# Kernel tuning notes

Measured on AMD Instinct MI355X. Metric: run time of the kernel, lower is better.

Reference implementation:

```python
import jax, jax.numpy as jnp
import numpy as np

N_NODES, N_EDGES, N_ROOTS = 32768, 131072, 1024
VOCAB, EMB_D, FEAT = 50000, 256, 128
SEQ, HEADS, OUT_CH = 16, 16, 125
KERNELS = (5, 6, 7, 8)


def _add_self_loops(edge_index, n):
    loop = jnp.arange(n, dtype=edge_index.dtype)
    src = jnp.concatenate([edge_index[0], loop])
    dst = jnp.concatenate([edge_index[1], loop])
    return src, dst


def _gat_conv(x, W, a_src, a_dst, b, src, dst, n):
    # PyG GATConv (heads=1): h=xW, e_ij = LeakyReLU(a_s.h_j + a_d.h_i), softmax over incoming edges of i
    h = x @ W                                   # [N, F]
    al_s = h @ a_src                            # [N]
    al_d = h @ a_dst                            # [N]
    e = jax.nn.leaky_relu(al_s[src] + al_d[dst], 0.2)   # [E+N]
    m = jax.ops.segment_max(e, dst, num_segments=n)
    ex = jnp.exp(e - m[dst])
    den = jax.ops.segment_sum(ex, dst, num_segments=n)
    coef = ex / den[dst]
    out = jax.ops.segment_sum(coef[:, None] * h[src], dst, num_segments=n)
    return out + b


def _gcn_conv(x, W, b, src, dst, n):
    h = x @ W
    ones = jnp.ones_like(src, dtype=x.dtype)
    deg = jax.ops.segment_sum(ones, dst, num_segments=n)
    dinv = jax.lax.rsqrt(jnp.maximum(deg, 1.0))
    norm = dinv[src] * dinv[dst]                # [E+N]
    out = jax.ops.segment_sum(norm[:, None] * h[src], dst, num_segments=n)
    return out + b


def _transformer_block(x, Wq, bq, Wk, bk, Wv, bv, Wo, bo, g, be):
    # multi-head self-attention + output proj + residual + layernorm (attn_dropout=0)
    n, s, d = x.shape
    dh = d // HEADS
    q = (x @ Wq + bq).reshape(n, s, HEADS, dh)
    k = (x @ Wk + bk).reshape(n, s, HEADS, dh)
    v = (x @ Wv + bv).reshape(n, s, HEADS, dh)
    att = jnp.einsum('nqhd,nkhd->nhqk', q, k) / np.sqrt(dh).astype(np.float32)
    att = jax.nn.softmax(att, axis=-1)
    o = jnp.einsum('nhqk,nkhd->nqhd', att, v).reshape(n, s, d)
    o = o @ Wo + bo
    y = x + o
    mu = jnp.mean(y, axis=-1, keepdims=True)
    var = jnp.var(y, axis=-1, keepdims=True)
    return (y - mu) * jax.lax.rsqrt(var + 1e-5) * g + be


def _conv_branch(t, ws, bs):
    # t: [N, D, S]; Conv1d VALID + ReLU + max-pool over full output length
    feats = []
    for w, b in zip(ws, bs):
        a = jax.lax.conv_general_dilated(t, w, (1,), 'VALID',
                                         dimension_numbers=('NCH', 'OIH', 'NCH'))
        a = jax.nn.relu(a + b[:, None])
        feats.append(jnp.max(a, axis=-1))       # [N, OUT_CH]
    return jnp.concatenate(feats, axis=1)        # [N, 4*OUT_CH]


def _forward(x2, emb, Wq, bq, Wk, bk, Wv, bv, Wo, bo, ln_g, ln_b,
             gat1_W, gat1_as, gat1_ad, gat1_b, gcn1_W, gcn1_b,
             gat2_W, gat2_as, gat2_ad, gat2_b, gcn2_W, gcn2_b,
             conv_w0, conv_b0, conv_w1, conv_b1, conv_w2, conv_b2, conv_w3, conv_b3,
             fc1_W, fc1_b, fc2_W, fc2_b,
             text2, edge_index, root_index, rootpost_index):
    n = x2.shape[0]
    src, dst = _add_self_loops(edge_index, n)

    stance_graph = _gat_conv(x2, gat1_W, gat1_as, gat1_ad, gat1_b, src, dst, n)
    stance_shared = _gcn_conv(x2, gcn1_W, gcn1_b, src, dst, n)

    t = emb[text2]                                            # [N, S, D]
    t = _transformer_block(t, Wq, bq, Wk, bk, Wv, bv, Wo, bo, ln_g, ln_b)
    t_avg = jnp.mean(t, axis=1)                               # [N, D]

    cat = jnp.concatenate([stance_graph, stance_shared, t_avg], axis=1)  # [N, 2F+D]
    stance_graph2 = _gat_conv(cat, gat2_W, gat2_as, gat2_ad, gat2_b, src, dst, n)
    _ = _gcn_conv(stance_shared, gcn2_W, gcn2_b, src, dst, n)  # computed but unused in forward (faithful)

    tc = jnp.transpose(t, (0, 2, 1))                          # [N, D, S]
    text_feat = _conv_branch(tc, (conv_w0, conv_w1, conv_w2, conv_w3),
                             (conv_b0, conv_b1, conv_b2, conv_b3))  # [N, 500]

    final = jnp.concatenate([stance_graph2[root_index],
                             text_feat[root_index],
                             text_feat[rootpost_index]], axis=1)     # [B, F+1000]
    h = jax.nn.relu(final @ fc1_W + fc1_b)
    return h @ fc2_W + fc2_b                                  # [B, 3]


def setup_inputs() -> dict:
    key = jax.random.key(0)
    ks = iter(jax.random.split(key, 48))
    s = 0.05
    inp = {}
    inp['x2'] = jax.random.normal(next(ks), (N_NODES, FEAT), jnp.float32)
    inp['emb'] = jax.random.normal(next(ks), (VOCAB, EMB_D), jnp.float32) * s
    for nm in ['Wq', 'Wk', 'Wv', 'Wo']:
        inp[nm] = jax.random.normal(next(ks), (EMB_D, EMB_D), jnp.float32) * s
    for nm in ['bq', 'bk', 'bv', 'bo']:
        inp[nm] = jnp.zeros((EMB_D,), jnp.float32)
    inp['ln_g'] = jnp.ones((EMB_D,), jnp.float32)
    inp['ln_b'] = jnp.zeros((EMB_D,), jnp.float32)
    inp['gat1_W'] = jax.random.normal(next(ks), (FEAT, FEAT), jnp.float32) * s
    inp['gat1_as'] = jax.random.normal(next(ks), (FEAT,), jnp.float32) * s
    inp['gat1_ad'] = jax.random.normal(next(ks), (FEAT,), jnp.float32) * s
    inp['gat1_b'] = jnp.zeros((FEAT,), jnp.float32)
    inp['gcn1_W'] = jax.random.normal(next(ks), (FEAT, FEAT), jnp.float32) * s
    inp['gcn1_b'] = jnp.zeros((FEAT,), jnp.float32)
    inp['gat2_W'] = jax.random.normal(next(ks), (2 * FEAT + EMB_D, FEAT), jnp.float32) * s
    inp['gat2_as'] = jax.random.normal(next(ks), (FEAT,), jnp.float32) * s
    inp['gat2_ad'] = jax.random.normal(next(ks), (FEAT,), jnp.float32) * s
    inp['gat2_b'] = jnp.zeros((FEAT,), jnp.float32)
    inp['gcn2_W'] = jax.random.normal(next(ks), (FEAT, FEAT), jnp.float32) * s
    inp['gcn2_b'] = jnp.zeros((FEAT,), jnp.float32)
    for i, K in enumerate(KERNELS):
        inp[f'conv_w{i}'] = jax.random.normal(next(ks), (OUT_CH, EMB_D, K), jnp.float32) * s
        inp[f'conv_b{i}'] = jnp.zeros((OUT_CH,), jnp.float32)
    inp['fc1_W'] = jax.random.normal(next(ks), (FEAT + 8 * OUT_CH, 300), jnp.float32) * s
    inp['fc1_b'] = jnp.zeros((300,), jnp.float32)
    inp['fc2_W'] = jax.random.normal(next(ks), (300, 3), jnp.float32) * s
    inp['fc2_b'] = jnp.zeros((3,), jnp.float32)
    inp['text2'] = jax.random.randint(next(ks), (N_NODES, SEQ), 0, VOCAB, jnp.int32)
    inp['edge_index'] = jax.random.randint(next(ks), (2, N_EDGES), 0, N_NODES, jnp.int32)
    inp['root_index'] = jax.random.randint(next(ks), (N_ROOTS,), 0, N_NODES, jnp.int32)
    inp['rootpost_index'] = jax.random.randint(next(ks), (N_ROOTS,), 0, N_NODES, jnp.int32)
    return inp


def reference(x2, emb, Wq, bq, Wk, bk, Wv, bv, Wo, bo, ln_g, ln_b,
              gat1_W, gat1_as, gat1_ad, gat1_b, gcn1_W, gcn1_b,
              gat2_W, gat2_as, gat2_ad, gat2_b, gcn2_W, gcn2_b,
              conv_w0, conv_b0, conv_w1, conv_b1, conv_w2, conv_b2, conv_w3, conv_b3,
              fc1_W, fc1_b, fc2_W, fc2_b,
              text2, edge_index, root_index, rootpost_index):
    return _forward(x2, emb, Wq, bq, Wk, bk, Wv, bv, Wo, bo, ln_g, ln_b,
                    gat1_W, gat1_as, gat1_ad, gat1_b, gcn1_W, gcn1_b,
                    gat2_W, gat2_as, gat2_ad, gat2_b, gcn2_W, gcn2_b,
                    conv_w0, conv_b0, conv_w1, conv_b1, conv_w2, conv_b2, conv_w3, conv_b3,
                    fc1_W, fc1_b, fc2_W, fc2_b,
                    text2, edge_index, root_index, rootpost_index)
```

## Files before the change

kernel.cpp:

```cpp
#include <hip/hip_runtime.h>
#include <hip/hip_bf16.h>
#include <cstdint>
#include <cstddef>

#define N_NODES 32768
#define N_EDGES 131072
#define ET_EDGES (N_EDGES + N_NODES)
#define N_ROOTS 1024
#define EMB_D 256
#define FEAT 128
#define SEQ 16
#define OUT_CH 125

static inline int cdiv(long long a, long long b) { return (int)((a + b - 1) / b); }

typedef short short8 __attribute__((ext_vector_type(8)));
typedef short short4v __attribute__((ext_vector_type(4)));
typedef float f32x4 __attribute__((ext_vector_type(4)));

__device__ __forceinline__ float warpReduceSum(float v) {
#pragma unroll
    for (int m = 32; m; m >>= 1) v += __shfl_xor(v, m, 64);
    return v;
}
__device__ __forceinline__ int encf(float f) {
    int i = __float_as_int(f);
    return i >= 0 ? i : (i ^ 0x7fffffff);
}
__device__ __forceinline__ float decf(int i) {
    return __int_as_float(i >= 0 ? i : (i ^ 0x7fffffff));
}
__device__ __forceinline__ short f2bs(float x) {
    unsigned u = __float_as_uint(x);
    u += 0x7fffu + ((u >> 16) & 1u);
    return (short)(u >> 16);
}
__device__ __forceinline__ short2 f2bs2(float a, float b) {
    union {
        __hip_bfloat162 h;
        short2 s;
    } u;
    u.h = __float22bfloat162_rn(make_float2(a, b));
    return u.s;
}
__device__ __forceinline__ float bs2f(short s) {
    return __uint_as_float(((unsigned)(unsigned short)s) << 16);
}

__global__ void fill_i32(int* p, int v, int n) {
    int i = blockIdx.x * 256 + threadIdx.x;
    if (i < n) p[i] = v;
}

__global__ void init_cat(float* __restrict__ cat, const float* __restrict__ b1, const float* __restrict__ b2) {
    int i = blockIdx.x * 256 + threadIdx.x;
    int n = i >> 8, c = i & 255;
    float b = (c < 128) ? b1[c] : b2[c - 128];
    cat[(size_t)n * 512 + c] = b;
}

__global__ void repack_wall(const float* __restrict__ cw0, const float* __restrict__ cw1,
                            const float* __restrict__ cw2, const float* __restrict__ cw3,
                            __hip_bfloat16* __restrict__ wall) {
    int i = blockIdx.x * 256 + threadIdx.x;
    if (i >= 512 * 2048) return;
    int r = i >> 11, c = i & 2047;
    int k = c >> 8, ic = c & 255;
    float v = 0.f;
    if (r < 500) {
        int Kidx = r / 125, oc = r - Kidx * 125;
        int K = 5 + Kidx;
        if (k < K) {
            const float* cw = Kidx == 0 ? cw0 : Kidx == 1 ? cw1 : Kidx == 2 ? cw2 : cw3;
            v = cw[((size_t)oc * 256 + ic) * K + k];
        }
    }
    wall[i] = __float2bfloat16(v);
}

__global__ void repack_xf(const float* __restrict__ Wq, const float* __restrict__ Wk, const float* __restrict__ Wv,
                          const float* __restrict__ Wo, const float* __restrict__ bq, const float* __restrict__ bk,
                          const float* __restrict__ bv, short* __restrict__ wqkvT, short* __restrict__ woT,
                          float* __restrict__ bqkv) {
    int i = blockIdx.x * 256 + threadIdx.x;
    if (i < 768 * 256) {
        int n = i >> 8, k = i & 255;
        const float* W = n < 256 ? Wq : n < 512 ? Wk : Wv;
        wqkvT[i] = f2bs(W[k * 256 + (n & 255)]);
    }
    if (i < 256 * 256) {
        int n = i >> 8, k = i & 255;
        woT[i] = f2bs(Wo[k * 256 + n]);
    }
    if (i < 768) bqkv[i] = i < 256 ? bq[i] : i < 512 ? bk[i - 256] : bv[i - 512];
}

__global__ void repack_wT(const float* __restrict__ W, short* __restrict__ out, int K, int N) {
    int i = blockIdx.x * 256 + threadIdx.x;
    if (i >= K * N) return;
    int n = i / K, k = i - n * K;
    out[i] = f2bs(W[(size_t)k * N + n]);
}

__global__ __launch_bounds__(256) void mfma_gemm_n128(const float* __restrict__ A, const short* __restrict__ Wt,
                                                      float* __restrict__ C, int K) {
    __shared__ short As[128 * 40];
    __shared__ short Bs[128 * 40];
    const int m0 = blockIdx.x * 128;
    const int tid = threadIdx.x;
    const int lane = tid & 63;
    const int wave = tid >> 6;
    const int wm = (wave >> 1) * 64, wn = (wave & 1) * 64;
    const int quad = lane >> 4, l16 = lane & 15;

    const int r0 = tid >> 2, kc = (tid & 3) * 8;
    const int r1 = r0 + 64;

    f32x4 acc[4][4];
#pragma unroll
    for (int i = 0; i < 4; i++)
#pragma unroll
        for (int j = 0; j < 4; j++) acc[i][j] = (f32x4){0.f, 0.f, 0.f, 0.f};

    for (int k0 = 0; k0 < K; k0 += 32) {
#pragma unroll
        for (int rr = 0; rr < 2; rr++) {
            const int r = rr ? r1 : r0;
            const float* pa = A + (size_t)(m0 + r) * K + k0 + kc;
            float4 a0 = ((const float4*)pa)[0], a1 = ((const float4*)pa)[1];
            short2 c0 = f2bs2(a0.x, a0.y), c1 = f2bs2(a0.z, a0.w), c2 = f2bs2(a1.x, a1.y), c3 = f2bs2(a1.z, a1.w);
            *(short8*)(As + r * 40 + kc) = (short8){c0.x, c0.y, c1.x, c1.y, c2.x, c2.y, c3.x, c3.y};
        }
        *(short8*)(Bs + r0 * 40 + kc) = *(const short8*)(Wt + (size_t)r0 * K + k0 + kc);
        *(short8*)(Bs + r1 * 40 + kc) = *(const short8*)(Wt + (size_t)r1 * K + k0 + kc);
        __syncthreads();
        short8 af[4], bfr[4];
#pragma unroll
        for (int i = 0; i < 4; i++) af[i] = *(const short8*)(As + (wm + i * 16 + l16) * 40 + quad * 8);
#pragma unroll
        for (int j = 0; j < 4; j++) bfr[j] = *(const short8*)(Bs + (wn + j * 16 + l16) * 40 + quad * 8);
#pragma unroll
        for (int i = 0; i < 4; i++)
#pragma unroll
            for (int j = 0; j < 4; j++)
                acc[i][j] = __builtin_amdgcn_mfma_f32_16x16x32_bf16(af[i], bfr[j], acc[i][j], 0, 0, 0);
        __syncthreads();
    }
#pragma unroll
    for (int i = 0; i < 4; i++) {
#pragma unroll
        for (int j = 0; j < 4; j++) {
            const int col = wn + j * 16 + l16;
            const size_t base = (size_t)(m0 + wm + i * 16 + quad * 4) * 128 + col;
#pragma unroll
            for (int r = 0; r < 4; r++) C[base + (size_t)r * 128] = acc[i][j][r];
        }
    }
}

__global__ __launch_bounds__(256) void gemm64(const float* __restrict__ A, const float* __restrict__ B,
                                              const float* __restrict__ bias, float* __restrict__ C,
                                              int M, int N, int K, int lda, int ldc, int doRelu) {
    __shared__ float As[16][65];
    __shared__ float Bs[16][65];
    const int bm = blockIdx.y * 64, bn = blockIdx.x * 64;
    const int tid = threadIdx.x;
    const int tx = tid & 15, ty = tid >> 4;
    float acc[4][4] = {};
    for (int k0 = 0; k0 < K; k0 += 16) {
#pragma unroll
        for (int j = 0; j < 4; j++) {
            int i = tid + j * 256;
            int kk = i & 15, m = i >> 4;
            int gr = bm + m, gc = k0 + kk;
            As[kk][m] = (gr < M && gc < K) ? A[(size_t)gr * lda + gc] : 0.f;
        }
#pragma unroll
        for (int j = 0; j < 4; j++) {
            int i = tid + j * 256;
            int n = i & 63, kk = i >> 6;
            int gr = k0 + kk, gc = bn + n;
            Bs[kk][n] = (gr < K && gc < N) ? B[(size_t)gr * N + gc] : 0.f;
        }
        __syncthreads();
#pragma unroll
        for (int kk = 0; kk < 16; kk++) {
            float a[4], b[4];
#pragma unroll
            for (int i2 = 0; i2 < 4; i2++) a[i2] = As[kk][ty * 4 + i2];
#pragma unroll
            for (int j2 = 0; j2 < 4; j2++) b[j2] = Bs[kk][tx * 4 + j2];
#pragma unroll
            for (int i2 = 0; i2 < 4; i2++)
#pragma unroll
                for (int j2 = 0; j2 < 4; j2++) acc[i2][j2] = fmaf(a[i2], b[j2], acc[i2][j2]);
        }
        __syncthreads();
    }
#pragma unroll
    for (int i2 = 0; i2 < 4; i2++) {
        int r = bm + ty * 4 + i2;
        if (r >= M) continue;
#pragma unroll
        for (int j2 = 0; j2 < 4; j2++) {
            int c = bn + tx * 4 + j2;
            if (c >= N) continue;
            float v = acc[i2][j2];
            if (bias) v += bias[c];
            if (doRelu) v = fmaxf(v, 0.f);
            C[(size_t)r * ldc + c] = v;
        }
    }
}

__global__ __launch_bounds__(256) void alpha_kernel(const float* __restrict__ h, const float* __restrict__ asrc,
                                                    const float* __restrict__ adst, float* __restrict__ als,
                                                    float* __restrict__ ald) {
    int gw = (blockIdx.x * 256 + threadIdx.x) >> 6;
    int lane = threadIdx.x & 63;
    if (gw >= N_NODES) return;
    const float* row = h + (size_t)gw * FEAT;
    float v0 = row[lane], v1 = row[lane + 64];
    float ps = v0 * asrc[lane] + v1 * asrc[lane + 64];
    float pd = v0 * adst[lane] + v1 * adst[lane + 64];
    ps = warpReduceSum(ps);
    pd = warpReduceSum(pd);
    if (lane == 0) {
        als[gw] = ps;
        ald[gw] = pd;
    }
}

__device__ __forceinline__ void edge_decode(int i, const int* __restrict__ ei, int& s, int& d) {
    if (i < N_EDGES) {
        s = ei[i];
        d = ei[N_EDGES + i];
    } else {
        s = d = i - N_EDGES;
    }
}

__global__ void edge_p1(const int* __restrict__ ei, const float* __restrict__ als, const float* __restrict__ ald,
                        float* __restrict__ elog, int* __restrict__ menc, float* dega) {
    int i = blockIdx.x * 256 + threadIdx.x;
    if (i >= ET_EDGES) return;
    int s, d;
    edge_decode(i, ei, s, d);
    float e = als[s] + ald[d];
    e = (e >= 0.f) ? e : 0.2f * e;
    elog[i] = e;
    atomicMax(&menc[d], encf(e));
    if (dega) unsafeAtomicAdd(&dega[d], 1.f);
}

__global__ void edge_p2(const int* __restrict__ ei, float* __restrict__ elog, const int* __restrict__ menc,
                        float* __restrict__ den) {
    int i = blockIdx.x * 256 + threadIdx.x;
    if (i >= ET_EDGES) return;
    int s, d;
    edge_decode(i, ei, s, d);
    float ex = __expf(elog[i] - decf(menc[d]));
    elog[i] = ex;
    unsafeAtomicAdd(&den[d], ex);
}

__global__ void edge_p2b(const int* __restrict__ ei, float* __restrict__ elog, const float* __restrict__ den) {
    int i = blockIdx.x * 256 + threadIdx.x;
    if (i >= ET_EDGES) return;
    int s, d;
    edge_decode(i, ei, s, d);
    elog[i] = elog[i] / den[d];
}

__global__ void dinv_kernel(float* deg) {
    int i = blockIdx.x * 256 + threadIdx.x;
    if (i < N_NODES) deg[i] = rsqrtf(fmaxf(deg[i], 1.f));
}

__global__ void edge_scatter(const int* __restrict__ ei, const float* __restrict__ coef, const float* __restrict__ h,
                             float* __restrict__ out, int ldo) {
    int i = blockIdx.x * 256 + threadIdx.x;
    if (i >= ET_EDGES * FEAT) return;
    int e = i >> 7, f = i & 127;
    int s, d;
    edge_decode(e, ei, s, d);
    unsafeAtomicAdd(&out[(size_t)d * ldo + f], coef[e] * h[(size_t)s * FEAT + f]);
}

__global__ void gcn_scatter(const int* __restrict__ ei, const float* __restrict__ dinv, const float* __restrict__ h,
                            float* __restrict__ out, int ldo) {
    int i = blockIdx.x * 256 + threadIdx.x;
    if (i >= ET_EDGES * FEAT) return;
    int e = i >> 7, f = i & 127;
    int s, d;
    edge_decode(e, ei, s, d);
    float coef = dinv[s] * dinv[d];
    unsafeAtomicAdd(&out[(size_t)d * ldo + f], coef * h[(size_t)s * FEAT + f]);
}

__global__ void root_gather(const float* __restrict__ g2, const int* __restrict__ rooti, const float* __restrict__ gb,
                            float* __restrict__ fin) {
    int i = blockIdx.x * 256 + threadIdx.x;
    if (i >= N_ROOTS * FEAT) return;
    int r = i >> 7, c = i & 127;
    fin[(size_t)r * 1128 + c] = g2[(size_t)rooti[r] * FEAT + c] + gb[c];
}

__global__ void fc2_kernel(const float* __restrict__ fch, const float* __restrict__ W, const float* __restrict__ b,
                           float* __restrict__ out) {
    int i = blockIdx.x * 256 + threadIdx.x;
    if (i >= N_ROOTS * 3) return;
    int r = i / 3, c = i - r * 3;
    float acc = b[c];
    for (int k = 0; k < 300; k++) acc = fmaf(fch[(size_t)r * 300 + k], W[k * 3 + c], acc);
    out[i] = acc;
}

#define QA_STRIDE 264
#define KR_STRIDE 264

__device__ __forceinline__ int vt_addr(int d, int key) {
    return d * 32 + (((key & 24) ^ (((d ^ (d >> 2)) & 3) << 3)) | (key & 7));
}

template <int MODE>
__global__ __launch_bounds__(256, 4) void xformer_kernel(
    const float* __restrict__ emb, const int* __restrict__ text2, const short* __restrict__ wqkvT,
    const float* __restrict__ bqkv, const short* __restrict__ woT, const float* __restrict__ bo,
    const float* __restrict__ lng, const float* __restrict__ lnb, const int* __restrict__ rooti,
    const int* __restrict__ rpi, float* __restrict__ cat, unsigned short* __restrict__ tbuf) {
    __shared__ short qa[32 * QA_STRIDE];
    __shared__ short kreg[32 * KR_STRIDE];

    const int tid = threadIdx.x;
    const int wave = tid >> 6, lane = tid & 63;
    const int quad = lane >> 4, l16 = lane & 15;

    int gnode[2];
#pragma unroll
    for (int m = 0; m < 2; m++) {
        int slot = blockIdx.x * 2 + m;
        gnode[m] = (MODE == 0) ? slot : ((slot < N_ROOTS) ? rooti[slot] : rpi[slot - N_ROOTS]);
    }
    const int tokA0 = text2[gnode[0] * SEQ + l16];
    const int tokA1 = text2[gnode[1] * SEQ + l16];

    short8 Areg[2][8];
#pragma unroll
    for (int k0 = 0; k0 < 8; k0++) {
        const float* pa0 = emb + (size_t)tokA0 * 256 + k0 * 32 + quad * 8;
        const float* pa1 = emb + (size_t)tokA1 * 256 + k0 * 32 + quad * 8;
        float4 a0l = ((const float4*)pa0)[0], a0h = ((const float4*)pa0)[1];
        float4 a1l = ((const float4*)pa1)[0], a1h = ((const float4*)pa1)[1];
        short2 c0 = f2bs2(a0l.x, a0l.y), c1 = f2bs2(a0l.z, a0l.w), c2 = f2bs2(a0h.x, a0h.y), c3 = f2bs2(a0h.z, a0h.w);
        Areg[0][k0] = (short8){c0.x, c0.y, c1.x, c1.y, c2.x, c2.y, c3.x, c3.y};
        c0 = f2bs2(a1l.x, a1l.y);
        c1 = f2bs2(a1l.z, a1l.w);
        c2 = f2bs2(a1h.x, a1h.y);
        c3 = f2bs2(a1h.z, a1h.w);
        Areg[1][k0] = (short8){c0.x, c0.y, c1.x, c1.y, c2.x, c2.y, c3.x, c3.y};
    }

    f32x4 vacc[4][2];

#pragma unroll
    for (int grp = 0; grp < 3; grp++) {
        f32x4 acc[4][2];
#pragma unroll
        for (int i = 0; i < 4; i++) {
            acc[i][0] = (f32x4){0.f, 0.f, 0.f, 0.f};
            acc[i][1] = (f32x4){0.f, 0.f, 0.f, 0.f};
        }
#pragma unroll
        for (int k0 = 0; k0 < 8; k0++) {
#pragma unroll
            for (int i = 0; i < 4; i++) {
                const int g = grp * 16 + wave * 4 + i;
                short8 B = *(const short8*)(wqkvT + (size_t)(g * 16 + l16) * 256 + k0 * 32 + quad * 8);
                acc[i][0] = __builtin_amdgcn_mfma_f32_16x16x32_bf16(Areg[0][k0], B, acc[i][0], 0, 0, 0);
                acc[i][1] = __builtin_amdgcn_mfma_f32_16x16x32_bf16(Areg[1][k0], B, acc[i][1], 0, 0, 0);
            }
        }
#pragma unroll
        for (int i = 0; i < 4; i++) {
            const int g = grp * 16 + wave * 4 + i;
            const int col = g * 16 + l16;
            const float b = bqkv[col];
            if (grp == 2) {
#pragma unroll
                for (int m = 0; m < 2; m++) {
                    vacc[i][m][0] = acc[i][m][0] + b;
                    vacc[i][m][1] = acc[i][m][1] + b;
                    vacc[i][m][2] = acc[i][m][2] + b;
                    vacc[i][m][3] = acc[i][m][3] + b;
                }
            } else {
#pragma unroll
                for (int m = 0; m < 2; m++) {
                    const int rbase = m * 16 + quad * 4;
                    float v0 = acc[i][m][0] + b, v1 = acc[i][m][1] + b;
                    float v2 = acc[i][m][2] + b, v3 = acc[i][m][3] + b;
                    if (grp == 0) {
                        v0 *= 0.25f;
                        v1 *= 0.25f;
                        v2 *= 0.25f;
                        v3 *= 0.25f;
                    }
                    short2 p01 = f2bs2(v0, v1), p23 = f2bs2(v2, v3);
                    short* dst = (grp == 0) ? (qa + rbase * QA_STRIDE + col) : (kreg + rbase * KR_STRIDE + (col - 256));
                    const int str = (grp == 0) ? QA_STRIDE : KR_STRIDE;
                    dst[0 * str] = p01.x;
                    dst[1 * str] = p01.y;
                    dst[2 * str] = p23.x;
                    dst[3 * str] = p23.y;
                }
            }
        }
    }

#pragma unroll
    for (int p = 0; p < 2; p++) {
#pragma unroll
        for (int i = 0; i < 4; i++) {
            const int h = wave * 4 + i;
            const int arow = p * 16 + l16;
            const int q8 = (quad & 1) * 8;
            short8 Af = *(const short8*)(kreg + arow * KR_STRIDE + h * 16 + q8);
            short8 Bf = *(const short8*)(qa + arow * QA_STRIDE + h * 16 + q8);
            if (quad >= 2) {
                Af = (short8){0, 0, 0, 0, 0, 0, 0, 0};
                Bf = (short8){0, 0, 0, 0, 0, 0, 0, 0};
            }
            f32x4 S = __builtin_amdgcn_mfma_f32_16x16x32_bf16(Af, Bf, (f32x4){0.f, 0.f, 0.f, 0.f}, 0, 0, 0);
            float mx = fmaxf(fmaxf(S[0], S[1]), fmaxf(S[2], S[3]));
            mx = fmaxf(mx, __shfl_xor(mx, 16));
            mx = fmaxf(mx, __shfl_xor(mx, 32));
            float e0 = __expf(S[0] - mx), e1 = __expf(S[1] - mx);
            float e2 = __expf(S[2] - mx), e3 = __expf(S[3] - mx);
            float sm = (e0 + e1) + (e2 + e3);
            sm += __shfl_xor(sm, 16);
            sm += __shfl_xor(sm, 32);
            const float inv = 1.f / sm;
            short2 p01 = f2bs2(e0 * inv, e1 * inv), p23 = f2bs2(e2 * inv, e3 * inv);
            *(short4v*)(qa + arow * QA_STRIDE + h * 16 + quad * 4) = (short4v){p01.x, p01.y, p23.x, p23.y};
        }
    }
    __syncthreads();

#pragma unroll
    for (int i = 0; i < 4; i++) {
        const int d = (wave * 4 + i) * 16 + l16;
#pragma unroll
        for (int m = 0; m < 2; m++) {
            const int rbase = m * 16 + quad * 4;
            short2 p01 = f2bs2(vacc[i][m][0], vacc[i][m][1]), p23 = f2bs2(vacc[i][m][2], vacc[i][m][3]);
            *(short4v*)(kreg + vt_addr(d, rbase)) = (short4v){p01.x, p01.y, p23.x, p23.y};
        }
    }

#pragma unroll
    for (int p = 0; p < 2; p++) {
#pragma unroll
        for (int i = 0; i < 4; i++) {
            const int h = wave * 4 + i;
            const int arow = p * 16 + l16;
            const int q8 = (quad & 1) * 8;
            short8 BP = *(const short8*)(qa + arow * QA_STRIDE + h * 16 + q8);
            short8 Av = *(const short8*)(kreg + vt_addr(h * 16 + l16, p * 16 + q8));
            if (quad >= 2) {
                BP = (short8){0, 0, 0, 0, 0, 0, 0, 0};
                Av = (short8){0, 0, 0, 0, 0, 0, 0, 0};
            }
            f32x4 O = __builtin_amdgcn_mfma_f32_16x16x32_bf16(Av, BP, (f32x4){0.f, 0.f, 0.f, 0.f}, 0, 0, 0);
            short2 o01 = f2bs2(O[0], O[1]), o23 = f2bs2(O[2], O[3]);
            *(short4v*)(qa + arow * QA_STRIDE + h * 16 + quad * 4) = (short4v){o01.x, o01.y, o23.x, o23.y};
        }
    }
    __syncthreads();

    {
        short8 Afr[2][8];
#pragma unroll
        for (int m = 0; m < 2; m++)
#pragma unroll
            for (int k0 = 0; k0 < 8; k0++)
                Afr[m][k0] = *(const short8*)(qa + (m * 16 + l16) * QA_STRIDE + k0 * 32 + quad * 8);
#pragma unroll
        for (int i = 0; i < 4; i++) {
            const int g = wave * 4 + i;
            f32x4 oa0 = (f32x4){0.f, 0.f, 0.f, 0.f}, oa1 = (f32x4){0.f, 0.f, 0.f, 0.f};
#pragma unroll
            for (int k0 = 0; k0 < 8; k0++) {
                short8 B = *(const short8*)(woT + (size_t)(g * 16 + l16) * 256 + k0 * 32 + quad * 8);
                oa0 = __builtin_amdgcn_mfma_f32_16x16x32_bf16(Afr[0][k0], B, oa0, 0, 0, 0);
                oa1 = __builtin_amdgcn_mfma_f32_16x16x32_bf16(Afr[1][k0], B, oa1, 0, 0, 0);
            }
            const int col = g * 16 + l16;
            const float bocol = bo[col];
            short2 a01 = f2bs2(oa0[0] + bocol, oa0[1] + bocol), a23 = f2bs2(oa0[2] + bocol, oa0[3] + bocol);
            short2 c01 = f2bs2(oa1[0] + bocol, oa1[1] + bocol), c23 = f2bs2(oa1[2] + bocol, oa1[3] + bocol);
            kreg[(quad * 4 + 0) * KR_STRIDE + col] = a01.x;
            kreg[(quad * 4 + 1) * KR_STRIDE + col] = a01.y;
            kreg[(quad * 4 + 2) * KR_STRIDE + col] = a23.x;
            kreg[(quad * 4 + 3) * KR_STRIDE + col] = a23.y;
            kreg[(16 + quad * 4 + 0) * KR_STRIDE + col] = c01.x;
            kreg[(16 + quad * 4 + 1) * KR_STRIDE + col] = c01.y;
            kreg[(16 + quad * 4 + 2) * KR_STRIDE + col] = c23.x;
            kreg[(16 + quad * 4 + 3) * KR_STRIDE + col] = c23.y;
        }
    }
    __syncthreads();

    float* qs = (float*)qa;
    {
        const int row = tid >> 3, seg = tid & 7;
        const int m = row >> 4, r = row & 15;
        const int tokr = text2[gnode[m] * SEQ + r];
        const float* ep = emb + (size_t)tokr * 256 + seg * 32;
        float sum = 0.f, sq = 0.f;
#pragma unroll
        for (int j = 0; j < 4; j++) {
            short8 y8 = *(const short8*)(kreg + row * KR_STRIDE + seg * 32 + j * 8);
            float4 ea = ((const float4*)(ep + j * 8))[0];
            float4 eb = ((const float4*)(ep + j * 8))[1];
            float ev[8] = {ea.x, ea.y, ea.z, ea.w, eb.x, eb.y, eb.z, eb.w};
            float yv[8];
#pragma unroll
            for (int e = 0; e < 8; e++) {
                yv[e] = bs2f(y8[e]) + ev[e];
                sum += yv[e];
                sq = fmaf(yv[e], yv[e], sq);
            }
            short2 w0 = f2bs2(yv[0], yv[1]), w1 = f2bs2(yv[2], yv[3]);
            short2 w2 = f2bs2(yv[4], yv[5]), w3 = f2bs2(yv[6], yv[7]);
            *(short4v*)(kreg + row * KR_STRIDE + seg * 32 + j * 8) = (short4v){w0.x, w0.y, w1.x, w1.y};
            *(short4v*)(kreg + row * KR_STRIDE + seg * 32 + j * 8 + 4) = (short4v){w2.x, w2.y, w3.x, w3.y};
        }
        qs[tid] = sum;
        qs[256 + tid] = sq;
    }
    __syncthreads();
    if (tid < 32) {
        float s = 0.f, q2 = 0.f;
#pragma unroll
        for (int j = 0; j < 8; j++) {
            s += qs[tid * 8 + j];
            q2 += qs[256 + tid * 8 + j];
        }
        float mu = s * (1.f / 256.f);
        float var = q2 * (1.f / 256.f) - mu * mu;
        qs[512 + tid * 2] = mu;
        qs[512 + tid * 2 + 1] = rsqrtf(var + 1e-5f);
    }
    __syncthreads();
    {
        const int c = tid;
        const float g = lng[c], bb = lnb[c];
        float csum[2] = {0.f, 0.f};
#pragma unroll
        for (int m = 0; m < 2; m++) {
#pragma unroll
            for (int r = 0; r < 16; r++) {
                const int row = m * 16 + r;
                const float yv = bs2f(kreg[row * KR_STRIDE + c]);
                const float mu = qs[512 + row * 2], rstd = qs[512 + row * 2 + 1];
                const float o = (yv - mu) * rstd * g + bb;
                if (MODE == 0) {
                    csum[m] += o;
                } else {
                    tbuf[((size_t)(blockIdx.x * 2 + m) * 24 + r) * 256 + c] = (unsigned short)f2bs(o);
                }
            }
        }
        if (MODE == 0) {
            cat[(size_t)gnode[0] * 512 + 256 + c] = csum[0] * (1.f / 16.f);
            cat[(size_t)gnode[1] * 512 + 256 + c] = csum[1] * (1.f / 16.f);
        } else {
            for (int z = tid; z < 2 * 8 * 256; z += 256) {
                const int m = z >> 11, rem = z & 2047;
                tbuf[((size_t)(blockIdx.x * 2 + m) * 24 + 16 + (rem >> 8)) * 256 + (rem & 255)] = 0;
            }
        }
    }
}

__global__ __launch_bounds__(256) void conv_gemm(const short* __restrict__ tb, const short* __restrict__ wall,
                                                 float* __restrict__ C) {
    __shared__ short As[128 * 40];
    __shared__ short Bs[128 * 40];
    const int bid = blockIdx.x;
    const int m0 = (bid >> 2) * 128;
    const int n0 = (bid & 3) * 128;
    const int tid = threadIdx.x;
    const int lane = tid & 63;
    const int wave = tid >> 6;
    const int wm = (wave >> 1) * 64, wn = (wave & 1) * 64;
    const int quad = lane >> 4, l16 = lane & 15;

    const int r0 = tid >> 2, kc = (tid & 3) * 8;
    const int r1 = r0 + 64;
    const int am0 = m0 + r0, am1 = m0 + r1;
    const int s0 = am0 / 12, p0_ = am0 - s0 * 12;
    const int s1 = am1 / 12, p1_ = am1 - s1 * 12;
    const size_t ga0 = (size_t)(s0 * 24 + p0_) * 256 + kc;
    const size_t ga1 = (size_t)(s1 * 24 + p1_) * 256 + kc;
    const size_t gb0 = (size_t)(n0 + r0) * 2048 + kc;
    const size_t gb1 = (size_t)(n0 + r1) * 2048 + kc;
    short* sa0 = As + r0 * 40 + kc;
    short* sa1 = As + r1 * 40 + kc;
    short* sb0 = Bs + r0 * 40 + kc;
    short* sb1 = Bs + r1 * 40 + kc;

    f32x4 acc[4][4];
#pragma unroll
    for (int i = 0; i < 4; i++)
#pragma unroll
        for (int j = 0; j < 4; j++) acc[i][j] = (f32x4){0.f, 0.f, 0.f, 0.f};

    for (int k0 = 0; k0 < 2048; k0 += 32) {
        short8 a0 = *(const short8*)(tb + ga0 + k0);
        short8 a1 = *(const short8*)(tb + ga1 + k0);
        short8 b0 = *(const short8*)(wall + gb0 + k0);
        short8 b1 = *(const short8*)(wall + gb1 + k0);
        *(short8*)sa0 = a0;
        *(short8*)sa1 = a1;
        *(short8*)sb0 = b0;
        *(short8*)sb1 = b1;
        __syncthreads();
        short8 af[4], bfr[4];
#pragma unroll
        for (int i = 0; i < 4; i++) af[i] = *(const short8*)(As + (wm + i * 16 + l16) * 40 + quad * 8);
#pragma unroll
        for (int j = 0; j < 4; j++) bfr[j] = *(const short8*)(Bs + (wn + j * 16 + l16) * 40 + quad * 8);
#pragma unroll
        for (int i = 0; i < 4; i++)
#pragma unroll
            for (int j = 0; j < 4; j++)
                acc[i][j] = __builtin_amdgcn_mfma_f32_16x16x32_bf16(af[i], bfr[j], acc[i][j], 0, 0, 0);
        __syncthreads();
    }
#pragma unroll
    for (int i = 0; i < 4; i++) {
#pragma unroll
        for (int j = 0; j < 4; j++) {
            const int col = n0 + wn + j * 16 + l16;
            const size_t base = (size_t)(m0 + wm + i * 16 + quad * 4) * 512 + col;
#pragma unroll
            for (int r = 0; r < 4; r++) C[base + (size_t)r * 512] = acc[i][j][r];
        }
    }
}

__global__ void conv_maxpool(const float* __restrict__ C, const float* __restrict__ cb0, const float* __restrict__ cb1,
                             const float* __restrict__ cb2, const float* __restrict__ cb3, float* __restrict__ fin) {
    int i = blockIdx.x * 256 + threadIdx.x;
    if (i >= 2048 * 500) return;
    int slot = i / 500, q = i - slot * 500;
    int Kidx = q / 125, oc = q - Kidx * 125;
    int L = 12 - Kidx;
    const float* base = C + (size_t)(slot * 12) * 512 + q;
    float m = base[0];
    for (int p = 1; p < L; p++) m = fmaxf(m, base[(size_t)p * 512]);
    float b = (Kidx == 0 ? cb0 : Kidx == 1 ? cb1 : Kidx == 2 ? cb2 : cb3)[oc];
    float v = fmaxf(m + b, 0.f);
    int idx = slot < N_ROOTS ? slot : slot - N_ROOTS;
    int colbase = slot < N_ROOTS ? 128 : 628;
    fin[(size_t)idx * 1128 + colbase + q] = v;
}

extern "C" void kernel_launch(void* const* d_in, const int* in_sizes, int n_in, void* d_out, int out_size, void* d_ws,
                              size_t ws_size, hipStream_t stream) {
    const float* x2 = (const float*)d_in[0];
    const float* emb = (const float*)d_in[1];
    const float* Wq = (const float*)d_in[2];
    const float* Wk = (const float*)d_in[3];
    const float* Wv = (const float*)d_in[4];
    const float* Wo = (const float*)d_in[5];
    const float* bq = (const float*)d_in[6];
    const float* bk = (const float*)d_in[7];
    const float* bv = (const float*)d_in[8];
    const float* bo = (const float*)d_in[9];
    const float* lng = (const float*)d_in[10];
    const float* lnb = (const float*)d_in[11];
    const float* gat1_W = (const float*)d_in[12];
    const float* gat1_as = (const float*)d_in[13];
    const float* gat1_ad = (const float*)d_in[14];
    const float* gat1_b = (const float*)d_in[15];
    const float* gcn1_W = (const float*)d_in[16];
    const float* gcn1_b = (const float*)d_in[17];
    const float* gat2_W = (const float*)d_in[18];
    const float* gat2_as = (const float*)d_in[19];
    const float* gat2_ad = (const float*)d_in[20];
    const float* gat2_b = (const float*)d_in[21];
    const float* cw0 = (const float*)d_in[24];
    const float* cb0 = (const float*)d_in[25];
    const float* cw1 = (const float*)d_in[26];
    const float* cb1 = (const float*)d_in[27];
    const float* cw2 = (const float*)d_in[28];
    const float* cb2 = (const float*)d_in[29];
    const float* cw3 = (const float*)d_in[30];
    const float* cb3 = (const float*)d_in[31];
    const float* fc1_W = (const float*)d_in[32];
    const float* fc1_b = (const float*)d_in[33];
    const float* fc2_W = (const float*)d_in[34];
    const float* fc2_b = (const float*)d_in[35];
    const int* text2 = (const int*)d_in[36];
    const int* ei = (const int*)d_in[37];
    const int* rooti = (const int*)d_in[38];
    const int* rpi = (const int*)d_in[39];

    float* ws = (float*)d_ws;
    size_t off = 0;
    auto alloc = [&](size_t n) {
        float* p = ws + off;
        off += n;
        return p;
    };
    float* g2o = alloc((size_t)N_NODES * FEAT);
    float* den1 = alloc(N_NODES);
    float* den2 = alloc(N_NODES);
    float* deg = alloc(N_NODES);
    size_t zero_floats = off;
    float* cat = alloc((size_t)N_NODES * 512);
    float* h1 = alloc((size_t)N_NODES * FEAT);
    float* h2 = alloc((size_t)N_NODES * FEAT);
    float* hg2 = alloc((size_t)N_NODES * FEAT);
    float* als1 = alloc(N_NODES);
    float* ald1 = alloc(N_NODES);
    float* als2 = alloc(N_NODES);
    float* ald2 = alloc(N_NODES);
    int* m1 = (int*)alloc(N_NODES);
    int* m2 = (int*)alloc(N_NODES);
    float* el1 = alloc(ET_EDGES);
    float* el2 = alloc(ET_EDGES);
    float* fin = alloc((size_t)N_ROOTS * 1128);
    float* fch = alloc((size_t)N_ROOTS * 300);
    float* wallf = alloc(512 * 2048 / 2);
    float* wqkvTf = alloc(768 * 256 / 2);
    float* woTf = alloc(256 * 256 / 2);
    float* bqkv = alloc(768);
    float* wg1Tf = alloc(128 * 128 / 2);
    float* wc1Tf = alloc(128 * 128 / 2);
    float* wg2Tf = alloc(128 * 512 / 2);
    (void)ws_size;
    (void)in_sizes;
    (void)n_in;
    (void)out_size;

    unsigned short* tbuf = (unsigned short*)h1;
    __hip_bfloat16* wall = (__hip_bfloat16*)wallf;
    short* wqkvT = (short*)wqkvTf;
    short* woT = (short*)woTf;
    short* wg1T = (short*)wg1Tf;
    short* wc1T = (short*)wc1Tf;
    short* wg2T = (short*)wg2Tf;
    float* Cbuf = cat;

    hipMemsetAsync(g2o, 0, zero_floats * sizeof(float), stream);
    init_cat<<<cdiv((long long)N_NODES * 256, 256), 256, 0, stream>>>(cat, gat1_b, gcn1_b);
    fill_i32<<<cdiv(2 * N_NODES, 256), 256, 0, stream>>>(m1, (int)0x80000000, 2 * N_NODES);
    repack_wall<<<cdiv(512 * 2048, 256), 256, 0, stream>>>(cw0, cw1, cw2, cw3, wall);
    repack_xf<<<cdiv(768 * 256, 256), 256, 0, stream>>>(Wq, Wk, Wv, Wo, bq, bk, bv, wqkvT, woT, bqkv);
    repack_wT<<<cdiv(128 * 128, 256), 256, 0, stream>>>(gat1_W, wg1T, 128, 128);
    repack_wT<<<cdiv(128 * 128, 256), 256, 0, stream>>>(gcn1_W, wc1T, 128, 128);
    repack_wT<<<cdiv(512 * 128, 256), 256, 0, stream>>>(gat2_W, wg2T, 512, 128);

    mfma_gemm_n128<<<N_NODES / 128, 256, 0, stream>>>(x2, wg1T, h1, 128);
    mfma_gemm_n128<<<N_NODES / 128, 256, 0, stream>>>(x2, wc1T, h2, 128);
    alpha_kernel<<<cdiv((long long)N_NODES * 64, 256), 256, 0, stream>>>(h1, gat1_as, gat1_ad, als1, ald1);
    edge_p1<<<cdiv(ET_EDGES, 256), 256, 0, stream>>>(ei, als1, ald1, el1, m1, deg);
    edge_p2<<<cdiv(ET_EDGES, 256), 256, 0, stream>>>(ei, el1, m1, den1);
    edge_p2b<<<cdiv(ET_EDGES, 256), 256, 0, stream>>>(ei, el1, den1);
    dinv_kernel<<<cdiv(N_NODES, 256), 256, 0, stream>>>(deg);
    const int sc_blocks = cdiv((long long)ET_EDGES * FEAT, 256);
    edge_scatter<<<sc_blocks, 256, 0, stream>>>(ei, el1, h1, cat + 0, 512);
    gcn_scatter<<<sc_blocks, 256, 0, stream>>>(ei, deg, h2, cat + 128, 512);
    xformer_kernel<0><<<N_NODES / 2, 256, 0, stream>>>(emb, text2, wqkvT, bqkv, woT, bo, lng, lnb, rooti, rpi, cat,
                                                       nullptr);
    xformer_kernel<1><<<2 * N_ROOTS / 2, 256, 0, stream>>>(emb, text2, wqkvT, bqkv, woT, bo, lng, lnb, rooti, rpi,
                                                           nullptr, tbuf);
    mfma_gemm_n128<<<N_NODES / 128, 256, 0, stream>>>(cat, wg2T, hg2, 512);
    alpha_kernel<<<cdiv((long long)N_NODES * 64, 256), 256, 0, stream>>>(hg2, gat2_as, gat2_ad, als2, ald2);
    edge_p1<<<cdiv(ET_EDGES, 256), 256, 0, stream>>>(ei, als2, ald2, el2, m2, nullptr);
    edge_p2<<<cdiv(ET_EDGES, 256), 256, 0, stream>>>(ei, el2, m2, den2);
    edge_p2b<<<cdiv(ET_EDGES, 256), 256, 0, stream>>>(ei, el2, den2);
    edge_scatter<<<sc_blocks, 256, 0, stream>>>(ei, el2, hg2, g2o, FEAT);
    conv_gemm<<<192 * 4, 256, 0, stream>>>((const short*)tbuf, (const short*)wall, Cbuf);
    root_gather<<<cdiv(N_ROOTS * FEAT, 256), 256, 0, stream>>>(g2o, rooti, gat2_b, fin);
    conv_maxpool<<<cdiv(2048 * 500, 256), 256, 0, stream>>>(Cbuf, cb0, cb1, cb2, cb3, fin);
    gemm64<<<dim3(cdiv(300, 64), cdiv(N_ROOTS, 64)), 256, 0, stream>>>(fin, fc1_W, fc1_b, fch, N_ROOTS, 300, 1128,
                                                                       1128, 300, 1);
    fc2_kernel<<<cdiv(N_ROOTS * 3, 256), 256, 0, stream>>>(fch, fc2_W, fc2_b, (float*)d_out);
}
```

Before: 2.184 ms.

## Stage embedding tile in LDS and software-pipeline weight loads in transformer GEMMs

The embedding rows are now converted to bf16 once, cooperatively and with coalesced loads, into shared memory, so each wave no longer holds a 2x8 short8 A-fragment array in registers. The QKV and output-projection GEMMs use a shared lambda that double-buffers the global weight fragments, loading the next k-slice while MFMAs run on the current one, and reads A fragments from LDS. The K projection is computed last so it can overwrite the embedding tile after a barrier. This is meant to cut register pressure and hide global load latency, at the cost of more LDS traffic and an extra barrier.

```diff
diff --git a/kernel.cpp b/kernel.cpp
--- a/kernel.cpp
+++ b/kernel.cpp
@@ -342,78 +342,99 @@
         int slot = blockIdx.x * 2 + m;
         gnode[m] = (MODE == 0) ? slot : ((slot < N_ROOTS) ? rooti[slot] : rpi[slot - N_ROOTS]);
     }
-    const int tokA0 = text2[gnode[0] * SEQ + l16];
-    const int tokA1 = text2[gnode[1] * SEQ + l16];
-
-    short8 Areg[2][8];
-#pragma unroll
-    for (int k0 = 0; k0 < 8; k0++) {
-        const float* pa0 = emb + (size_t)tokA0 * 256 + k0 * 32 + quad * 8;
-        const float* pa1 = emb + (size_t)tokA1 * 256 + k0 * 32 + quad * 8;
-        float4 a0l = ((const float4*)pa0)[0], a0h = ((const float4*)pa0)[1];
-        float4 a1l = ((const float4*)pa1)[0], a1h = ((const float4*)pa1)[1];
-        short2 c0 = f2bs2(a0l.x, a0l.y), c1 = f2bs2(a0l.z, a0l.w), c2 = f2bs2(a0h.x, a0h.y), c3 = f2bs2(a0h.z, a0h.w);
-        Areg[0][k0] = (short8){c0.x, c0.y, c1.x, c1.y, c2.x, c2.y, c3.x, c3.y};
-        c0 = f2bs2(a1l.x, a1l.y);
-        c1 = f2bs2(a1l.z, a1l.w);
-        c2 = f2bs2(a1h.x, a1h.y);
-        c3 = f2bs2(a1h.z, a1h.w);
-        Areg[1][k0] = (short8){c0.x, c0.y, c1.x, c1.y, c2.x, c2.y, c3.x, c3.y};
-    }
-
-    f32x4 vacc[4][2];
-
-#pragma unroll
-    for (int grp = 0; grp < 3; grp++) {
-        f32x4 acc[4][2];
+
+    {
+        const int row = tid >> 3, seg = tid & 7;
+        const int m = row >> 4, r = row & 15;
+        const int tok = text2[gnode[m] * SEQ + r];
+        const float* ep = emb + (size_t)tok * 256 + seg * 32;
+#pragma unroll
+        for (int j = 0; j < 4; j++) {
+            float4 ea = ((const float4*)(ep + j * 8))[0];
+            float4 eb = ((const float4*)(ep + j * 8))[1];
+            short2 w0 = f2bs2(ea.x, ea.y), w1 = f2bs2(ea.z, ea.w);
+            short2 w2 = f2bs2(eb.x, eb.y), w3 = f2bs2(eb.z, eb.w);
+            *(short8*)(kreg + row * KR_STRIDE + seg * 32 + j * 8) =
+                (short8){w0.x, w0.y, w1.x, w1.y, w2.x, w2.y, w3.x, w3.y};
+        }
+    }
+    __syncthreads();
+
+    auto run_gemm = [&](const short* __restrict__ W, int wrow0, const short* __restrict__ Albase,
+                        f32x4(&acc)[4][2]) {
 #pragma unroll
         for (int i = 0; i < 4; i++) {
             acc[i][0] = (f32x4){0.f, 0.f, 0.f, 0.f};
             acc[i][1] = (f32x4){0.f, 0.f, 0.f, 0.f};
         }
+        const short* wb = W + (size_t)(wrow0 + l16) * 256 + quad * 8;
+        short8 Bcur[4], Bnxt[4];
+#pragma unroll
+        for (int i = 0; i < 4; i++) Bcur[i] = *(const short8*)(wb + (size_t)i * 16 * 256);
 #pragma unroll
         for (int k0 = 0; k0 < 8; k0++) {
+            if (k0 < 7) {
+#pragma unroll
+                for (int i = 0; i < 4; i++)
+                    Bnxt[i] = *(const short8*)(wb + (size_t)i * 16 * 256 + (k0 + 1) * 32);
+            }
+            short8 A0 = *(const short8*)(Albase + l16 * KR_STRIDE + k0 * 32 + quad * 8);
+            short8 A1 = *(const short8*)(Albase + (16 + l16) * KR_STRIDE + k0 * 32 + quad * 8);
 #pragma unroll
             for (int i = 0; i < 4; i++) {
-                const int g = grp * 16 + wave * 4 + i;
-                short8 B = *(const short8*)(wqkvT + (size_t)(g * 16 + l16) * 256 + k0 * 32 + quad * 8);
-                acc[i][0] = __builtin_amdgcn_mfma_f32_16x16x32_bf16(Areg[0][k0], B, acc[i][0], 0, 0, 0);
-                acc[i][1] = __builtin_amdgcn_mfma_f32_16x16x32_bf16(Areg[1][k0], B, acc[i][1], 0, 0, 0);
-            }
-        }
+                acc[i][0] = __builtin_amdgcn_mfma_f32_16x16x32_bf16(A0, Bcur[i], acc[i][0], 0, 0, 0);
+                acc[i][1] = __builtin_amdgcn_mfma_f32_16x16x32_bf16(A1, Bcur[i], acc[i][1], 0, 0, 0);
+            }
+#pragma unroll
+            for (int i = 0; i < 4; i++) Bcur[i] = Bnxt[i];
+        }
+    };
+
+    f32x4 vacc[4][2];
+    {
+        f32x4 acc[4][2];
+        run_gemm(wqkvT, (0 * 16 + wave * 4) * 16, kreg, acc);
 #pragma unroll
         for (int i = 0; i < 4; i++) {
-            const int g = grp * 16 + wave * 4 + i;
-            const int col = g * 16 + l16;
+            const int col = (wave * 4 + i) * 16 + l16;
             const float b = bqkv[col];
-            if (grp == 2) {
-#pragma unroll
-                for (int m = 0; m < 2; m++) {
-                    vacc[i][m][0] = acc[i][m][0] + b;
-                    vacc[i][m][1] = acc[i][m][1] + b;
-                    vacc[i][m][2] = acc[i][m][2] + b;
-                    vacc[i][m][3] = acc[i][m][3] + b;
-                }
-            } else {
-#pragma unroll
-                for (int m = 0; m < 2; m++) {
-                    const int rbase = m * 16 + quad * 4;
-                    float v0 = acc[i][m][0] + b, v1 = acc[i][m][1] + b;
-                    float v2 = acc[i][m][2] + b, v3 = acc[i][m][3] + b;
-                    if (grp == 0) {
-                        v0 *= 0.25f;
-                        v1 *= 0.25f;
-                        v2 *= 0.25f;
-                        v3 *= 0.25f;
-                    }
-                    short2 p01 = f2bs2(v0, v1), p23 = f2bs2(v2, v3);
-                    short* dst = (grp == 0) ? (qa + rbase * QA_STRIDE + col) : (kreg + rbase * KR_STRIDE + (col - 256));
-                    const int str = (grp == 0) ? QA_STRIDE : KR_STRIDE;
-                    dst[0 * str] = p01.x;
-                    dst[1 * str] = p01.y;
-                    dst[2 * str] = p23.x;
-                    dst[3 * str] = p23.y;
-                }
+#pragma unroll
+            for (int m = 0; m < 2; m++) {
+                const int rbase = m * 16 + quad * 4;
+                short2 p01 = f2bs2((acc[i][m][0] + b) * 0.25f, (acc[i][m][1] + b) * 0.25f);
+                short2 p23 = f2bs2((acc[i][m][2] + b) * 0.25f, (acc[i][m][3] + b) * 0.25f);
+                qa[(rbase + 0) * QA_STRIDE + col] = p01.x;
+                qa[(rbase + 1) * QA_STRIDE + col] = p01.y;
+                qa[(rbase + 2) * QA_STRIDE + col] = p23.x;
+                qa[(rbase + 3) * QA_STRIDE + col] = p23.y;
+            }
+        }
+        run_gemm(wqkvT, (2 * 16 + wave * 4) * 16, kreg, vacc);
+#pragma unroll
+        for (int i = 0; i < 4; i++) {
+            const float b = bqkv[(2 * 16 + wave * 4 + i) * 16 + l16];
+#pragma unroll
+            for (int m = 0; m < 2; m++)
+#pragma unroll
+                for (int r = 0; r < 4; r++) vacc[i][m][r] += b;
+        }
+        f32x4 kacc[4][2];
+        run_gemm(wqkvT, (1 * 16 + wave * 4) * 16, kreg, kacc);
+        __syncthreads();
+#pragma unroll
+        for (int i = 0; i < 4; i++) {
+            const int colg = (1 * 16 + wave * 4 + i) * 16 + l16;
+            const float b = bqkv[colg];
+            const int cl = colg - 256;
+#pragma unroll
+            for (int m = 0; m < 2; m++) {
+                const int rbase = m * 16 + quad * 4;
+                short2 p01 = f2bs2(kacc[i][m][0] + b, kacc[i][m][1] + b);
+                short2 p23 = f2bs2(kacc[i][m][2] + b, kacc[i][m][3] + b);
+                kreg[(rbase + 0) * KR_STRIDE + cl] = p01.x;
+                kreg[(rbase + 1) * KR_STRIDE + cl] = p01.y;
+                kreg[(rbase + 2) * KR_STRIDE + cl] = p23.x;
+                kreg[(rbase + 3) * KR_STRIDE + cl] = p23.y;
             }
         }
     }
@@ -479,34 +500,22 @@
     __syncthreads();
 
     {
-        short8 Afr[2][8];
-#pragma unroll
-        for (int m = 0; m < 2; m++)
-#pragma unroll
-            for (int k0 = 0; k0 < 8; k0++)
-                Afr[m][k0] = *(const short8*)(qa + (m * 16 + l16) * QA_STRIDE + k0 * 32 + quad * 8);
+        f32x4 oacc[4][2];
+        run_gemm(woT, (wave * 4) * 16, qa, oacc);
 #pragma unroll
         for (int i = 0; i < 4; i++) {
-            const int g = wave * 4 + i;
-            f32x4 oa0 = (f32x4){0.f, 0.f, 0.f, 0.f}, oa1 = (f32x4){0.f, 0.f, 0.f, 0.f};
-#pragma unroll
-            for (int k0 = 0; k0 < 8; k0++) {
-                short8 B = *(const short8*)(woT + (size_t)(g * 16 + l16) * 256 + k0 * 32 + quad * 8);
-                oa0 = __builtin_amdgcn_mfma_f32_16x16x32_bf16(Afr[0][k0], B, oa0, 0, 0, 0);
-                oa1 = __builtin_amdgcn_mfma_f32_16x16x32_bf16(Afr[1][k0], B, oa1, 0, 0, 0);
-            }
-            const int col = g * 16 + l16;
+            const int col = (wave * 4 + i) * 16 + l16;
             const float bocol = bo[col];
-            short2 a01 = f2bs2(oa0[0] + bocol, oa0[1] + bocol), a23 = f2bs2(oa0[2] + bocol, oa0[3] + bocol);
-            short2 c01 = f2bs2(oa1[0] + bocol, oa1[1] + bocol), c23 = f2bs2(oa1[2] + bocol, oa1[3] + bocol);
-            kreg[(quad * 4 + 0) * KR_STRIDE + col] = a01.x;
-            kreg[(quad * 4 + 1) * KR_STRIDE + col] = a01.y;
-            kreg[(quad * 4 + 2) * KR_STRIDE + col] = a23.x;
-            kreg[(quad * 4 + 3) * KR_STRIDE + col] = a23.y;
-            kreg[(16 + quad * 4 + 0) * KR_STRIDE + col] = c01.x;
-            kreg[(16 + quad * 4 + 1) * KR_STRIDE + col] = c01.y;
-            kreg[(16 + quad * 4 + 2) * KR_STRIDE + col] = c23.x;
-            kreg[(16 + quad * 4 + 3) * KR_STRIDE + col] = c23.y;
+#pragma unroll
+            for (int m = 0; m < 2; m++) {
+                const int rbase = m * 16 + quad * 4;
+                short2 a01 = f2bs2(oacc[i][m][0] + bocol, oacc[i][m][1] + bocol);
+                short2 a23 = f2bs2(oacc[i][m][2] + bocol, oacc[i][m][3] + bocol);
+                kreg[(rbase + 0) * KR_STRIDE + col] = a01.x;
+                kreg[(rbase + 1) * KR_STRIDE + col] = a01.y;
+                kreg[(rbase + 2) * KR_STRIDE + col] = a23.x;
+                kreg[(rbase + 3) * KR_STRIDE + col] = a23.y;
+            }
         }
     }
     __syncthreads();
```

After: 2.100 ms. 1.04x faster.
